# Kernel optimization log

Hardware: AMD Instinct MI355X
Metric: run time of the kernel (lower is better)

The kernel has to match this reference:

```python
import jax, jax.numpy as jnp
import numpy as np

H = 512      # hidden_size
NH = 8       # head_size (num heads)
DH = H // NH # att_size per head
FFN = 2048
B, S = 8, 1024
NEG = -1e9
EPS = 1e-5


def _layernorm(x, g, b):
    mu = jnp.mean(x, axis=-1, keepdims=True)
    var = jnp.var(x, axis=-1, keepdims=True)
    return (x - mu) * jax.lax.rsqrt(var + EPS) * g + b


def setup_inputs() -> dict:
    key = jax.random.key(0)
    ks = jax.random.split(key, 16)
    s = 0.02
    return {
        "x": jax.random.normal(ks[0], (B, S, H), jnp.float32),
        "attn_bias": jax.random.normal(ks[1], (B, S, S), jnp.float32),
        "graph_mask": jax.random.randint(ks[2], (B, S, S), 0, 2, jnp.int32),
        "ln1_g": jnp.ones((H,), jnp.float32),
        "ln1_b": jnp.zeros((H,), jnp.float32),
        "Wq": jax.random.normal(ks[3], (H, H), jnp.float32) * s,
        "bq": jnp.zeros((H,), jnp.float32),
        "Wk": jax.random.normal(ks[4], (H, H), jnp.float32) * s,
        "bk": jnp.zeros((H,), jnp.float32),
        "Wv": jax.random.normal(ks[5], (H, H), jnp.float32) * s,
        "bv": jnp.zeros((H,), jnp.float32),
        "Wo": jax.random.normal(ks[6], (H, H), jnp.float32) * s,
        "bo": jnp.zeros((H,), jnp.float32),
        "ln2_g": jnp.ones((H,), jnp.float32),
        "ln2_b": jnp.zeros((H,), jnp.float32),
        "W1": jax.random.normal(ks[7], (H, FFN), jnp.float32) * s,
        "b1": jnp.zeros((FFN,), jnp.float32),
        "W2": jax.random.normal(ks[8], (FFN, H), jnp.float32) * s,
        "b2": jnp.zeros((H,), jnp.float32),
    }


def reference(x, attn_bias, graph_mask, ln1_g, ln1_b, Wq, bq, Wk, bk, Wv, bv,
              Wo, bo, ln2_g, ln2_b, W1, b1, W2, b2):
    b, s, h = x.shape
    # --- self-attention block (eval mode: dropouts are identity) ---
    y = _layernorm(x, ln1_g, ln1_b)
    q = (y @ Wq + bq).reshape(b, s, NH, DH).transpose(0, 2, 1, 3)  # [B,h,S,d]
    k = (y @ Wk + bk).reshape(b, s, NH, DH).transpose(0, 2, 1, 3)
    v = (y @ Wv + bv).reshape(b, s, NH, DH).transpose(0, 2, 1, 3)
    scale = DH ** -0.5
    scores = jnp.einsum('bhqd,bhkd->bhqk', q * scale, k)  # [B,h,S,S]
    mask = (graph_mask == 0)[:, None, :, :]               # [B,1,S,S] broadcast over heads
    bias = jnp.where(mask, NEG, attn_bias[:, None, :, :])
    scores = scores + bias
    scores = jnp.where(mask, NEG, scores)
    p = jax.nn.softmax(scores, axis=-1)
    o = jnp.einsum('bhqk,bhkd->bhqd', p, v)
    o = o.transpose(0, 2, 1, 3).reshape(b, s, h) @ Wo + bo
    x = x + o
    # --- FFN block ---
    y = _layernorm(x, ln2_g, ln2_b)
    y = jax.nn.gelu(y @ W1 + b1, approximate=False) @ W2 + b2
    return x + y
```

## Files before the change

### kernel.cpp

```cpp
#include <hip/hip_runtime.h>
#include <hip/hip_bf16.h>
#include <type_traits>

static constexpr int kS   = 1024;
static constexpr int kH   = 512;
static constexpr int kFFN = 2048;

using bf16 = __hip_bfloat16;
using short8  = __attribute__((ext_vector_type(8))) short;
using float4v = __attribute__((ext_vector_type(4))) float;
#define MFMA16 __builtin_amdgcn_mfma_f32_16x16x32_bf16

__device__ __forceinline__ unsigned short f2bfu(float f){
  unsigned int u = __float_as_uint(f);
  return (unsigned short)((u + 0x7fffu + ((u >> 16) & 1u)) >> 16);
}
__device__ __forceinline__ float bfu2f(unsigned short u){
  return __uint_as_float(((unsigned int)u) << 16);
}
__device__ __forceinline__ unsigned int pack2(float a, float b){
  return (unsigned int)f2bfu(a) | ((unsigned int)f2bfu(b) << 16);
}
__device__ __forceinline__ void async16(const void* g, void* l){
  __builtin_amdgcn_global_load_lds(
    (const __attribute__((address_space(1))) unsigned int*)g,
    (__attribute__((address_space(3))) unsigned int*)l, 16, 0, 0);
}
__device__ __forceinline__ int swz(int col, int row){
  return (col & ~63) | (((((col>>3)&7) ^ (row&7)))<<3) | (col&7);
}

__device__ __forceinline__ void ln_row(const float* __restrict__ x,
    const float* __restrict__ g, const float* __restrict__ bb,
    bf16* __restrict__ y, long row, int lane){
  const float* xr = x + row * kH + lane*8;
  float4 a = *(const float4*)xr, c = *(const float4*)(xr+4);
  float v[8] = {a.x,a.y,a.z,a.w,c.x,c.y,c.z,c.w};
  float s=0.f, s2=0.f;
#pragma unroll
  for(int i=0;i<8;i++){ s += v[i]; s2 += v[i]*v[i]; }
#pragma unroll
  for(int o=32; o>=1; o>>=1){ s += __shfl_xor(s,o,64); s2 += __shfl_xor(s2,o,64); }
  float mu  = s * (1.f/kH);
  float rs  = rsqrtf(s2*(1.f/kH) - mu*mu + 1e-5f);
  float gv[8], bv[8];
  {
    float4 t0=*(const float4*)(g+lane*8),  t1=*(const float4*)(g+lane*8+4);
    float4 t2=*(const float4*)(bb+lane*8), t3=*(const float4*)(bb+lane*8+4);
    gv[0]=t0.x;gv[1]=t0.y;gv[2]=t0.z;gv[3]=t0.w;gv[4]=t1.x;gv[5]=t1.y;gv[6]=t1.z;gv[7]=t1.w;
    bv[0]=t2.x;bv[1]=t2.y;bv[2]=t2.z;bv[3]=t2.w;bv[4]=t3.x;bv[5]=t3.y;bv[6]=t3.z;bv[7]=t3.w;
  }
  unsigned int ow[4];
#pragma unroll
  for(int i=0;i<4;i++){
    float a0 = (v[2*i]  -mu)*rs*gv[2*i]   + bv[2*i];
    float a1 = (v[2*i+1]-mu)*rs*gv[2*i+1] + bv[2*i+1];
    ow[i] = pack2(a0, a1);
  }
  *reinterpret_cast<uint4*>(y + row*kH + swz(lane*8, (int)row)) = make_uint4(ow[0],ow[1],ow[2],ow[3]);
}

__global__ __launch_bounds__(256) void ln_kernel(const float* __restrict__ x,
    const float* __restrict__ g, const float* __restrict__ bb, bf16* __restrict__ y){
  ln_row(x, g, bb, y, (long)blockIdx.x*4 + (threadIdx.x>>6), threadIdx.x&63);
}

__device__ __forceinline__ void prep_tile(const float* __restrict__ W,
    bf16* __restrict__ WT, int K, int N, int kb, int nb){
  __shared__ unsigned short Ts[64*68];
  int tid=threadIdx.x;
  {
    int k=tid>>2, nc=(tid&3)*16;
    const float* p = W + (size_t)(kb+k)*N + nb+nc;
#pragma unroll
    for(int i=0;i<16;i+=4){
      float4 f = *(const float4*)(p+i);
      Ts[k*68+nc+i  ]=f2bfu(f.x); Ts[k*68+nc+i+1]=f2bfu(f.y);
      Ts[k*68+nc+i+2]=f2bfu(f.z); Ts[k*68+nc+i+3]=f2bfu(f.w);
    }
  }
  __syncthreads();
  {
    int n=tid>>2, kc=(tid&3)*16;
    unsigned short tmp[16];
#pragma unroll
    for(int i=0;i<16;i++) tmp[i] = Ts[(kc+i)*68 + n];
    int row = nb+n, kg0 = kc>>3;
    bf16* op = WT + (size_t)row*K + kb;
    *(uint4*)(op + (((kg0  ^(row&7)))<<3)) = *(uint4*)&tmp[0];
    *(uint4*)(op + ((((kg0+1)^(row&7)))<<3)) = *(uint4*)&tmp[8];
  }
}

__global__ __launch_bounds__(256) void ln1_prep_qkv(
    const float* __restrict__ x, const float* __restrict__ g, const float* __restrict__ bb,
    bf16* __restrict__ y, const float* __restrict__ Wq, const float* __restrict__ Wk,
    const float* __restrict__ Wv, bf16* __restrict__ WT){
  int id = blockIdx.x;
  if(id < 2048){
    ln_row(x, g, bb, y, (long)id*4 + (threadIdx.x>>6), threadIdx.x&63);
  } else {
    int pid = id - 2048, sel = pid>>6, lid = pid&63;
    const float* W = sel==0 ? Wq : (sel==1 ? Wk : Wv);
    prep_tile(W, WT + (size_t)sel*262144, kH, kH, (lid>>3)*64, (lid&7)*64);
  }
}

__global__ __launch_bounds__(256) void prep_rest(
    const float* __restrict__ Wo, const float* __restrict__ W1, const float* __restrict__ W2,
    bf16* __restrict__ WoT, bf16* __restrict__ W1T, bf16* __restrict__ W2T){
  int id = blockIdx.x;
  const float* W; bf16* WT; int K, N, kb, nb;
  if(id < 64)       { W=Wo; WT=WoT; K=kH;   N=kH;   kb=(id>>3)*64;        nb=(id&7)*64; }
  else if(id < 320) { int l=id-64;  W=W1; WT=W1T; K=kH;   N=kFFN; kb=(l>>5)*64; nb=(l&31)*64; }
  else              { int l=id-320; W=W2; WT=W2T; K=kFFN; N=kH;   kb=(l>>3)*64; nb=(l&7)*64; }
  prep_tile(W, WT, K, N, kb, nb);
}

__global__ __launch_bounds__(256) void bias_eff_kernel(
    const int* __restrict__ mask, const float* __restrict__ bias, bf16* __restrict__ be){
  size_t i8 = ((size_t)blockIdx.x*256 + threadIdx.x)*8;
  int4   m0 = *(const int4*)(mask+i8),   m1 = *(const int4*)(mask+i8+4);
  float4 b0 = *(const float4*)(bias+i8), b1 = *(const float4*)(bias+i8+4);
  const unsigned short NEG = f2bfu(-1e9f);
  unsigned short o[8];
  o[0]=m0.x?f2bfu(b0.x):NEG; o[1]=m0.y?f2bfu(b0.y):NEG;
  o[2]=m0.z?f2bfu(b0.z):NEG; o[3]=m0.w?f2bfu(b0.w):NEG;
  o[4]=m1.x?f2bfu(b1.x):NEG; o[5]=m1.y?f2bfu(b1.y):NEG;
  o[6]=m1.z?f2bfu(b1.z):NEG; o[7]=m1.w?f2bfu(b1.w):NEG;
  *(uint4*)((unsigned short*)be + i8) = *(uint4*)o;
}

__global__ __launch_bounds__(256, 4) void quad_gemm(
    const bf16* __restrict__ A, const bf16* __restrict__ BT,
    const float* __restrict__ bias, const float* __restrict__ res,
    float* __restrict__ C, int M, int N, int K)
{
  __shared__ __align__(16) unsigned short As[2][64*64];
  __shared__ __align__(16) unsigned short Bs[2][64*64];
  int tid=threadIdx.x, lane=tid&63, quad=lane>>4, l16=lane&15;
  int w=__builtin_amdgcn_readfirstlane(tid>>6);
  int wr=w>>1, wc=w&1;
  int m0=blockIdx.y*64, n0=blockIdx.x*64;
  int lr=lane>>3, lc=lane&7;
  float4v acc[2][2]={};
  auto stage=[&](int k0,int bi){
#pragma unroll
    for(int i=0;i<2;i++){
      int r=(w*2+i)*8;
      async16(A  + (size_t)(m0+r+lr)*K + k0 + lc*8, &As[bi][r*64]);
      async16(BT + (size_t)(n0+r+lr)*K + k0 + lc*8, &Bs[bi][r*64]);
    }
  };
  stage(0,0);
  __syncthreads();
  int NT = K>>6;
  for(int kt=0;kt<NT;kt++){
    int cur=kt&1;
    if(kt+1<NT) stage((kt+1)<<6, cur^1);
#pragma unroll
    for(int hf=0;hf<2;hf++){
      short8 af[2], bfv[2];
#pragma unroll
      for(int mi=0;mi<2;mi++){
        int row=wr*32+mi*16+l16;
        af[mi]=*(const short8*)&As[cur][row*64 + (((hf*4+quad)^(row&7))<<3)];
      }
#pragma unroll
      for(int ni=0;ni<2;ni++){
        int n=wc*32+ni*16+l16;
        bfv[ni]=*(const short8*)&Bs[cur][n*64 + (((hf*4+quad)^(n&7))<<3)];
      }
#pragma unroll
      for(int ni=0;ni<2;ni++)
#pragma unroll
        for(int mi=0;mi<2;mi++)
          acc[mi][ni]=MFMA16(af[mi],bfv[ni],acc[mi][ni],0,0,0);
    }
    __syncthreads();
  }
#pragma unroll
  for(int ni=0;ni<2;ni++){
    int col=n0+wc*32+ni*16+l16;
    float bc=bias[col];
#pragma unroll
    for(int mi=0;mi<2;mi++){
#pragma unroll
      for(int r=0;r<4;r++){
        int row=m0+wr*32+mi*16+quad*4+r;
        float v=acc[mi][ni][r]+bc;
        size_t idx=(size_t)row*N+col;
        v+=res[idx];
        C[idx]=v;
      }
    }
  }
}

__global__ __launch_bounds__(256, 4) void quad_gelu(
    const bf16* __restrict__ A, const bf16* __restrict__ BT,
    const float* __restrict__ bias, bf16* __restrict__ C, int M, int N, int K)
{
  __shared__ __align__(16) unsigned short As[2][64*64];
  __shared__ __align__(16) unsigned short Bs[2][64*64];
  int tid=threadIdx.x, lane=tid&63, quad=lane>>4, l16=lane&15;
  int w=__builtin_amdgcn_readfirstlane(tid>>6);
  int wr=w>>1, wc=w&1;
  int m0=blockIdx.y*64, n0=blockIdx.x*64;
  int lr=lane>>3, lc=lane&7;
  float4v acc[2][2]={};
  auto stage=[&](int k0,int bi){
#pragma unroll
    for(int i=0;i<2;i++){
      int r=(w*2+i)*8;
      async16(A  + (size_t)(m0+r+lr)*K + k0 + lc*8, &As[bi][r*64]);
      async16(BT + (size_t)(n0+r+lr)*K + k0 + lc*8, &Bs[bi][r*64]);
    }
  };
  stage(0,0);
  __syncthreads();
  int NT = K>>6;
  for(int kt=0;kt<NT;kt++){
    int cur=kt&1;
    if(kt+1<NT) stage((kt+1)<<6, cur^1);
#pragma unroll
    for(int hf=0;hf<2;hf++){
      short8 af[2], bfv[2];
#pragma unroll
      for(int mi=0;mi<2;mi++){
        int row=wr*32+mi*16+l16;
        af[mi]=*(const short8*)&As[cur][row*64 + (((hf*4+quad)^(row&7))<<3)];
      }
#pragma unroll
      for(int ni=0;ni<2;ni++){
        int n=wc*32+ni*16+l16;
        bfv[ni]=*(const short8*)&Bs[cur][n*64 + (((hf*4+quad)^(n&7))<<3)];
      }
#pragma unroll
      for(int ni=0;ni<2;ni++)
#pragma unroll
        for(int mi=0;mi<2;mi++)
          acc[mi][ni]=MFMA16(af[mi],bfv[ni],acc[mi][ni],0,0,0);
    }
    __syncthreads();
  }
#pragma unroll
  for(int ni=0;ni<2;ni++){
    int col=n0+wc*32+ni*16+l16;
    float bc=bias[col];
#pragma unroll
    for(int mi=0;mi<2;mi++){
#pragma unroll
      for(int r=0;r<4;r++){
        int row=m0+wr*32+mi*16+quad*4+r;
        float v=acc[mi][ni][r]+bc;
        v=0.5f*v*(1.f+erff(v*0.70710678118f));
        reinterpret_cast<unsigned short*>(C)[(size_t)row*N + swz(col,row)]=f2bfu(v);
      }
    }
  }
}

__global__ __launch_bounds__(256, 3) void mfma_gemm_qkv(
    const bf16* __restrict__ A, const bf16* __restrict__ BT,
    const float* __restrict__ bq, const float* __restrict__ bk, const float* __restrict__ bv,
    bf16* __restrict__ qo, bf16* __restrict__ ko, bf16* __restrict__ vT, int M, int N, int K)
{
  __shared__ __align__(16) unsigned short As[128*64];
  __shared__ __align__(16) unsigned short Bs[128*64];
  int tid=threadIdx.x, lane=tid&63, quad=lane>>4, l16=lane&15;
  int w=__builtin_amdgcn_readfirstlane(tid>>6);
  int wr = w >> 1, wc = w & 1;
  int m0=blockIdx.y*128, n0=blockIdx.x*128;
  int lr=lane>>3, lc=lane&7;
  float4v acc[4][4] = {};
  for(int k0=0;k0<K;k0+=64){
    __syncthreads();
#pragma unroll
    for(int i=0;i<4;i++){
      int r = (w*4+i)*8;
      async16(A + (size_t)(m0+r+lr)*K + k0 + lc*8, &As[r*64]);
    }
#pragma unroll
    for(int i=0;i<4;i++){
      int r = (w*4+i)*8;
      async16(BT + (size_t)(n0+r+lr)*K + k0 + lc*8, &Bs[r*64]);
    }
    __syncthreads();
#pragma unroll
    for(int hf=0;hf<2;hf++){
      short8 af[4], bfv[4];
#pragma unroll
      for(int mi=0;mi<4;mi++){
        int row=wr*64+mi*16+l16;
        af[mi]=*(const short8*)&As[row*64 + (((hf*4+quad)^(row&7))<<3)];
      }
#pragma unroll
      for(int ni=0;ni<4;ni++){
        int n=wc*64+ni*16+l16;
        bfv[ni]=*(const short8*)&Bs[n*64 + (((hf*4+quad)^(n&7))<<3)];
      }
#pragma unroll
      for(int ni=0;ni<4;ni++)
#pragma unroll
        for(int mi=0;mi<4;mi++)
          acc[mi][ni]=MFMA16(af[mi],bfv[ni],acc[mi][ni],0,0,0);
    }
  }
  int sec = __builtin_amdgcn_readfirstlane(n0 >> 9);
  const float* bp = sec==0 ? bq : (sec==1 ? bk : bv);
  if(sec == 2){
#pragma unroll
    for(int ni=0;ni<4;ni++){
      int cl=(n0+wc*64+ni*16+l16)&511;
      float bc=bp[cl];
#pragma unroll
      for(int mi=0;mi<4;mi++){
        int row0=m0+wr*64+mi*16+quad*4;
        unsigned int p0=pack2(acc[mi][ni][0]+bc, acc[mi][ni][1]+bc);
        unsigned int p1=pack2(acc[mi][ni][2]+bc, acc[mi][ni][3]+bc);
        *reinterpret_cast<uint2*>(reinterpret_cast<unsigned short*>(vT)
            + (size_t)cl*8192 + row0) = make_uint2(p0,p1);
      }
    }
  } else {
    unsigned short* dst = (unsigned short*)(sec==0 ? qo : ko);
    float scl = (sec==0) ? 0.125f : 1.0f;
#pragma unroll
    for(int ni=0;ni<4;ni++){
      int col=n0+wc*64+ni*16+l16, cl=col&511;
      float bc=bp[cl];
#pragma unroll
      for(int mi=0;mi<4;mi++){
#pragma unroll
        for(int r=0;r<4;r++){
          int row=m0+wr*64+mi*16+quad*4+r;
          dst[(size_t)row*512+cl]=f2bfu((acc[mi][ni][r]+bc)*scl);
        }
      }
    }
  }
}

__global__ __launch_bounds__(256,2) void attn_mfma(
    const bf16* __restrict__ q, const bf16* __restrict__ k,
    const bf16* __restrict__ vT, const bf16* __restrict__ be,
    bf16* __restrict__ o)
{
  __shared__ __align__(16) unsigned short Ks[2][64*64];
  __shared__ __align__(16) unsigned short Vt[2][64*64];
  __shared__ __align__(16) unsigned short Ps[4*32*72];
  int tid=threadIdx.x, lane=tid&63, quad=lane>>4, l16=lane&15;
  int w=__builtin_amdgcn_readfirstlane(tid>>6);
  int lin = blockIdx.x;
  int nid = (lin&7)*64 + (lin>>3);
  int q0=(nid&7)*128, bh=nid>>3, b=bh>>3, h=bh&7;
  int lr=lane>>3, lc=lane&7;
  short8 aq[2][2];
#pragma unroll
  for(int g=0;g<2;g++){
    const bf16* qp = q + (size_t)(b*kS + q0 + w*32 + g*16 + l16)*kH + h*64;
    aq[g][0] = *(const short8*)(qp + quad*8);
    aq[g][1] = *(const short8*)(qp + 32 + quad*8);
  }
  float lpart[2][4]={};
  float4v oacc[2][4]={};
  int pb = w*32*72;
  const unsigned short* beRow[2][4];
#pragma unroll
  for(int g=0;g<2;g++)
#pragma unroll
    for(int r=0;r<4;r++)
      beRow[g][r] = reinterpret_cast<const unsigned short*>(be)
                  + (size_t)(b*kS+q0+w*32+g*16+quad*4+r)*kS + l16;

  auto stage = [&](int kt, int bufi){
    int kb = kt*64;
#pragma unroll
    for(int i=0;i<2;i++){
      int rr = w*16 + i*8;
      async16(k  + (size_t)(b*kS+kb+rr+lr)*kH + h*64 + ((lc^lr)<<3), &Ks[bufi][rr*64]);
      async16(vT + (size_t)(h*64+rr+lr)*8192 + b*kS + kb + ((lc^lr)<<3), &Vt[bufi][rr*64]);
    }
  };
  float bevc[2][4][4];
  stage(0,0);
#pragma unroll
  for(int g=0;g<2;g++)
#pragma unroll
    for(int r=0;r<4;r++)
#pragma unroll
      for(int t=0;t<4;t++)
        bevc[g][r][t] = bfu2f(beRow[g][r][t*16]);
  __syncthreads();
  for(int kt=0;kt<16;kt++){
    int cur=kt&1;
    if(kt<15) stage(kt+1, cur^1);
    float4v sa[2][4];
#pragma unroll
    for(int t=0;t<4;t++){
      int krow=t*16+l16, kx=krow&7;
      short8 b0 = *(const short8*)&Ks[cur][krow*64 + ((quad^kx)<<3)];
      short8 b1 = *(const short8*)&Ks[cur][krow*64 + (((4+quad)^kx)<<3)];
#pragma unroll
      for(int g=0;g<2;g++){
        float4v ci;
#pragma unroll
        for(int r=0;r<4;r++) ci[r] = bevc[g][r][t];
        ci = MFMA16(aq[g][0],b0,ci,0,0,0);
        sa[g][t]=MFMA16(aq[g][1],b1,ci,0,0,0);
      }
    }
    if(kt<15){
      int kb2=(kt+1)*64;
#pragma unroll
      for(int g=0;g<2;g++)
#pragma unroll
        for(int r=0;r<4;r++)
#pragma unroll
          for(int t=0;t<4;t++)
            bevc[g][r][t] = bfu2f(beRow[g][r][kb2 + t*16]);
    }
#pragma unroll
    for(int g=0;g<2;g++)
#pragma unroll
    for(int t=0;t<4;t++){
      int kg = t*2 + (l16>>3), j = l16&7;
#pragma unroll
      for(int r=0;r<4;r++){
        float p = __expf(sa[g][t][r] - 24.f);
        lpart[g][r] += p;
        int row = g*16 + quad*4+r;
        Ps[pb + row*72 + ((kg^(row&7))<<3) + j] = f2bfu(p);
      }
    }
    short8 ap[2][2];
#pragma unroll
    for(int g=0;g<2;g++){
      int prow = g*16 + l16;
      ap[g][0] = *(const short8*)&Ps[pb + prow*72 + ((quad^(prow&7))<<3)];
      ap[g][1] = *(const short8*)&Ps[pb + prow*72 + (((4+quad)^(prow&7))<<3)];
    }
#pragma unroll
    for(int dt=0;dt<4;dt++){
      int vrow=dt*16+l16, vx=vrow&7;
      short8 bv0=*(const short8*)&Vt[cur][vrow*64+((quad^vx)<<3)];
      short8 bv1=*(const short8*)&Vt[cur][vrow*64+(((4+quad)^vx)<<3)];
#pragma unroll
      for(int g=0;g<2;g++){
        oacc[g][dt]=MFMA16(ap[g][0],bv0,oacc[g][dt],0,0,0);
        oacc[g][dt]=MFMA16(ap[g][1],bv1,oacc[g][dt],0,0,0);
      }
    }
    __syncthreads();
  }
#pragma unroll
  for(int g=0;g<2;g++){
    float inv[4];
#pragma unroll
    for(int r=0;r<4;r++){
      float l = lpart[g][r];
      l += __shfl_xor(l,1,64); l += __shfl_xor(l,2,64);
      l += __shfl_xor(l,4,64); l += __shfl_xor(l,8,64);
      inv[r] = 1.f/l;
    }
#pragma unroll
    for(int dt=0;dt<4;dt++)
#pragma unroll
      for(int r=0;r<4;r++){
        int row = b*kS + q0 + w*32 + g*16 + quad*4 + r;
        int col = h*64 + dt*16 + l16;
        reinterpret_cast<unsigned short*>(o)[(size_t)row*kH + swz(col,row)] =
          f2bfu(oacc[g][dt][r]*inv[r]);
      }
  }
}

extern "C" void kernel_launch(void* const* d_in, const int* in_sizes, int n_in,
                              void* d_out, int out_size, void* d_ws, size_t ws_size,
                              hipStream_t stream){
  (void)in_sizes; (void)n_in; (void)out_size; (void)ws_size;
  const float* x         = (const float*)d_in[0];
  const float* attn_bias = (const float*)d_in[1];
  const int*   graph_mask= (const int*)  d_in[2];
  const float* ln1_g = (const float*)d_in[3];
  const float* ln1_b = (const float*)d_in[4];
  const float* Wq = (const float*)d_in[5];
  const float* bq = (const float*)d_in[6];
  const float* Wk = (const float*)d_in[7];
  const float* bk = (const float*)d_in[8];
  const float* Wv = (const float*)d_in[9];
  const float* bv = (const float*)d_in[10];
  const float* Wo = (const float*)d_in[11];
  const float* bo = (const float*)d_in[12];
  const float* ln2_g = (const float*)d_in[13];
  const float* ln2_b = (const float*)d_in[14];
  const float* W1 = (const float*)d_in[15];
  const float* b1 = (const float*)d_in[16];
  const float* W2 = (const float*)d_in[17];
  const float* b2 = (const float*)d_in[18];

  char* wsb = (char*)d_ws;
  const size_t SZ = (size_t)8192 * kH * sizeof(bf16);
  bf16* s0 = (bf16*)(wsb);
  bf16* s1 = (bf16*)(wsb + SZ);
  bf16* s2 = (bf16*)(wsb + 2*SZ);
  bf16* s3 = (bf16*)(wsb + 3*SZ);
  float* outf = (float*)d_out;
  bf16*  WqkvT = (bf16*)d_out;
  bf16*  beP   = (bf16*)d_out;
  bf16* WoT = s3;
  bf16* W1T = s3 + 262144;
  bf16* W2T = s3 + 262144 + 1048576;

  dim3 blk(256);
  ln1_prep_qkv<<<dim3(2240), blk, 0, stream>>>(x, ln1_g, ln1_b, s0, Wq, Wk, Wv, WqkvT);
  mfma_gemm_qkv<<<dim3(12,64), blk, 0, stream>>>(s0, WqkvT, bq, bk, bv, s1, s2, s3, 8192, 3*kH, kH);
  bias_eff_kernel<<<dim3(4096), blk, 0, stream>>>(graph_mask, attn_bias, beP);
  attn_mfma<<<dim3(512), blk, 0, stream>>>(s1, s2, s3, beP, s0);
  prep_rest<<<dim3(576), blk, 0, stream>>>(Wo, W1, W2, WoT, W1T, W2T);
  quad_gemm<<<dim3(8,128), blk, 0, stream>>>(s0, WoT, bo, x, outf, 8192, kH, kH);
  ln_kernel<<<dim3(2048), blk, 0, stream>>>(outf, ln2_g, ln2_b, s0);
  for(int c=0;c<2;c++){
    size_t ro = (size_t)c * 4096 * kH;
    quad_gelu<<<dim3(32,64), blk, 0, stream>>>(s0 + ro, W1T, b1, s1, 4096, kFFN, kH);
    quad_gemm<<<dim3(8,64),  blk, 0, stream>>>(s1, W2T, b2, outf + ro, outf + ro, 4096, kH, kFFN);
  }
}
```

Before: 338.9 us.

## Shrink QKV and FFN2 GEMM tiles with double-buffered LDS for more blocks

The QKV projection moves from a single-buffered 128x128 tile kernel to a 64x64 tile kernel with double-buffered async LDS staging. This quadruples the grid and lets the next K-tile load overlap with the MFMAs. The FFN down-projection gets a new 32x64-tile kernel so its 4096-row chunks launch twice as many blocks, improving CU fill for the long K=2048 loop. The cost is less operand reuse per block and more global/L2 traffic for the B operand.

```diff
diff --git a/kernel.cpp b/kernel.cpp
--- a/kernel.cpp
+++ b/kernel.cpp
@@ -197,6 +197,61 @@
   }
 }
 
+__global__ __launch_bounds__(256, 4) void quad32_gemm(
+    const bf16* __restrict__ A, const bf16* __restrict__ BT,
+    const float* __restrict__ bias, const float* __restrict__ res,
+    float* __restrict__ C, int M, int N, int K)
+{
+  __shared__ __align__(16) unsigned short As[2][32*64];
+  __shared__ __align__(16) unsigned short Bs[2][64*64];
+  int tid=threadIdx.x, lane=tid&63, quad=lane>>4, l16=lane&15;
+  int w=__builtin_amdgcn_readfirstlane(tid>>6);
+  int wr=w>>1, wc=w&1;
+  int m0=blockIdx.y*32, n0=blockIdx.x*64;
+  int lr=lane>>3, lc=lane&7;
+  float4v acc[2]={};
+  auto stage=[&](int k0,int bi){
+#pragma unroll
+    for(int i=0;i<3;i++){
+      int g=w*3+i;
+      if(g<4) async16(A  + (size_t)(m0+g*8+lr)*K     + k0 + lc*8, &As[bi][g*8*64]);
+      else    async16(BT + (size_t)(n0+(g-4)*8+lr)*K + k0 + lc*8, &Bs[bi][(g-4)*8*64]);
+    }
+  };
+  stage(0,0);
+  __syncthreads();
+  int NT = K>>6;
+  for(int kt=0;kt<NT;kt++){
+    int cur=kt&1;
+    if(kt+1<NT) stage((kt+1)<<6, cur^1);
+#pragma unroll
+    for(int hf=0;hf<2;hf++){
+      int row=wr*16+l16;
+      short8 af=*(const short8*)&As[cur][row*64 + (((hf*4+quad)^(row&7))<<3)];
+#pragma unroll
+      for(int ni=0;ni<2;ni++){
+        int n=wc*32+ni*16+l16;
+        short8 bfv=*(const short8*)&Bs[cur][n*64 + (((hf*4+quad)^(n&7))<<3)];
+        acc[ni]=MFMA16(af,bfv,acc[ni],0,0,0);
+      }
+    }
+    __syncthreads();
+  }
+#pragma unroll
+  for(int ni=0;ni<2;ni++){
+    int col=n0+wc*32+ni*16+l16;
+    float bc=bias[col];
+#pragma unroll
+    for(int r=0;r<4;r++){
+      int row=m0+wr*16+quad*4+r;
+      float v=acc[ni][r]+bc;
+      size_t idx=(size_t)row*N+col;
+      v+=res[idx];
+      C[idx]=v;
+    }
+  }
+}
+
 __global__ __launch_bounds__(256, 4) void quad_gelu(
     const bf16* __restrict__ A, const bf16* __restrict__ BT,
     const float* __restrict__ bias, bf16* __restrict__ C, int M, int N, int K)
@@ -261,62 +316,64 @@
   }
 }
 
-__global__ __launch_bounds__(256, 3) void mfma_gemm_qkv(
+__global__ __launch_bounds__(256, 4) void quad_qkv(
     const bf16* __restrict__ A, const bf16* __restrict__ BT,
     const float* __restrict__ bq, const float* __restrict__ bk, const float* __restrict__ bv,
     bf16* __restrict__ qo, bf16* __restrict__ ko, bf16* __restrict__ vT, int M, int N, int K)
 {
-  __shared__ __align__(16) unsigned short As[128*64];
-  __shared__ __align__(16) unsigned short Bs[128*64];
+  __shared__ __align__(16) unsigned short As[2][64*64];
+  __shared__ __align__(16) unsigned short Bs[2][64*64];
   int tid=threadIdx.x, lane=tid&63, quad=lane>>4, l16=lane&15;
   int w=__builtin_amdgcn_readfirstlane(tid>>6);
-  int wr = w >> 1, wc = w & 1;
-  int m0=blockIdx.y*128, n0=blockIdx.x*128;
+  int wr=w>>1, wc=w&1;
+  int m0=blockIdx.y*64, n0=blockIdx.x*64;
   int lr=lane>>3, lc=lane&7;
-  float4v acc[4][4] = {};
-  for(int k0=0;k0<K;k0+=64){
+  float4v acc[2][2]={};
+  auto stage=[&](int k0,int bi){
+#pragma unroll
+    for(int i=0;i<2;i++){
+      int r=(w*2+i)*8;
+      async16(A  + (size_t)(m0+r+lr)*K + k0 + lc*8, &As[bi][r*64]);
+      async16(BT + (size_t)(n0+r+lr)*K + k0 + lc*8, &Bs[bi][r*64]);
+    }
+  };
+  stage(0,0);
+  __syncthreads();
+  int NT = K>>6;
+  for(int kt=0;kt<NT;kt++){
+    int cur=kt&1;
+    if(kt+1<NT) stage((kt+1)<<6, cur^1);
+#pragma unroll
+    for(int hf=0;hf<2;hf++){
+      short8 af[2], bfv[2];
+#pragma unroll
+      for(int mi=0;mi<2;mi++){
+        int row=wr*32+mi*16+l16;
+        af[mi]=*(const short8*)&As[cur][row*64 + (((hf*4+quad)^(row&7))<<3)];
+      }
+#pragma unroll
+      for(int ni=0;ni<2;ni++){
+        int n=wc*32+ni*16+l16;
+        bfv[ni]=*(const short8*)&Bs[cur][n*64 + (((hf*4+quad)^(n&7))<<3)];
+      }
+#pragma unroll
+      for(int ni=0;ni<2;ni++)
+#pragma unroll
+        for(int mi=0;mi<2;mi++)
+          acc[mi][ni]=MFMA16(af[mi],bfv[ni],acc[mi][ni],0,0,0);
+    }
     __syncthreads();
-#pragma unroll
-    for(int i=0;i<4;i++){
-      int r = (w*4+i)*8;
-      async16(A + (size_t)(m0+r+lr)*K + k0 + lc*8, &As[r*64]);
-    }
-#pragma unroll
-    for(int i=0;i<4;i++){
-      int r = (w*4+i)*8;
-      async16(BT + (size_t)(n0+r+lr)*K + k0 + lc*8, &Bs[r*64]);
-    }
-    __syncthreads();
-#pragma unroll
-    for(int hf=0;hf<2;hf++){
-      short8 af[4], bfv[4];
-#pragma unroll
-      for(int mi=0;mi<4;mi++){
-        int row=wr*64+mi*16+l16;
-        af[mi]=*(const short8*)&As[row*64 + (((hf*4+quad)^(row&7))<<3)];
-      }
-#pragma unroll
-      for(int ni=0;ni<4;ni++){
-        int n=wc*64+ni*16+l16;
-        bfv[ni]=*(const short8*)&Bs[n*64 + (((hf*4+quad)^(n&7))<<3)];
-      }
-#pragma unroll
-      for(int ni=0;ni<4;ni++)
-#pragma unroll
-        for(int mi=0;mi<4;mi++)
-          acc[mi][ni]=MFMA16(af[mi],bfv[ni],acc[mi][ni],0,0,0);
-    }
-  }
-  int sec = __builtin_amdgcn_readfirstlane(n0 >> 9);
+  }
+  int sec = __builtin_amdgcn_readfirstlane((int)blockIdx.x >> 3);
   const float* bp = sec==0 ? bq : (sec==1 ? bk : bv);
   if(sec == 2){
 #pragma unroll
-    for(int ni=0;ni<4;ni++){
-      int cl=(n0+wc*64+ni*16+l16)&511;
+    for(int ni=0;ni<2;ni++){
+      int cl=(n0+wc*32+ni*16+l16)&511;
       float bc=bp[cl];
 #pragma unroll
-      for(int mi=0;mi<4;mi++){
-        int row0=m0+wr*64+mi*16+quad*4;
+      for(int mi=0;mi<2;mi++){
+        int row0=m0+wr*32+mi*16+quad*4;
         unsigned int p0=pack2(acc[mi][ni][0]+bc, acc[mi][ni][1]+bc);
         unsigned int p1=pack2(acc[mi][ni][2]+bc, acc[mi][ni][3]+bc);
         *reinterpret_cast<uint2*>(reinterpret_cast<unsigned short*>(vT)
@@ -327,14 +384,14 @@
     unsigned short* dst = (unsigned short*)(sec==0 ? qo : ko);
     float scl = (sec==0) ? 0.125f : 1.0f;
 #pragma unroll
-    for(int ni=0;ni<4;ni++){
-      int col=n0+wc*64+ni*16+l16, cl=col&511;
+    for(int ni=0;ni<2;ni++){
+      int col=n0+wc*32+ni*16+l16, cl=col&511;
       float bc=bp[cl];
 #pragma unroll
-      for(int mi=0;mi<4;mi++){
+      for(int mi=0;mi<2;mi++){
 #pragma unroll
         for(int r=0;r<4;r++){
-          int row=m0+wr*64+mi*16+quad*4+r;
+          int row=m0+wr*32+mi*16+quad*4+r;
           dst[(size_t)row*512+cl]=f2bfu((acc[mi][ni][r]+bc)*scl);
         }
       }
@@ -515,7 +572,7 @@
 
   dim3 blk(256);
   ln1_prep_qkv<<<dim3(2240), blk, 0, stream>>>(x, ln1_g, ln1_b, s0, Wq, Wk, Wv, WqkvT);
-  mfma_gemm_qkv<<<dim3(12,64), blk, 0, stream>>>(s0, WqkvT, bq, bk, bv, s1, s2, s3, 8192, 3*kH, kH);
+  quad_qkv<<<dim3(24,128), blk, 0, stream>>>(s0, WqkvT, bq, bk, bv, s1, s2, s3, 8192, 3*kH, kH);
   bias_eff_kernel<<<dim3(4096), blk, 0, stream>>>(graph_mask, attn_bias, beP);
   attn_mfma<<<dim3(512), blk, 0, stream>>>(s1, s2, s3, beP, s0);
   prep_rest<<<dim3(576), blk, 0, stream>>>(Wo, W1, W2, WoT, W1T, W2T);
@@ -523,7 +580,7 @@
   ln_kernel<<<dim3(2048), blk, 0, stream>>>(outf, ln2_g, ln2_b, s0);
   for(int c=0;c<2;c++){
     size_t ro = (size_t)c * 4096 * kH;
-    quad_gelu<<<dim3(32,64), blk, 0, stream>>>(s0 + ro, W1T, b1, s1, 4096, kFFN, kH);
-    quad_gemm<<<dim3(8,64),  blk, 0, stream>>>(s1, W2T, b2, outf + ro, outf + ro, 4096, kH, kFFN);
-  }
-}
+    quad_gelu <<<dim3(32,64),  blk, 0, stream>>>(s0 + ro, W1T, b1, s1, 4096, kFFN, kH);
+    quad32_gemm<<<dim3(8,128), blk, 0, stream>>>(s1, W2T, b2, outf + ro, outf + ro, 4096, kH, kFFN);
+  }
+}
```

Result: faster. 331.0 us (-2.4%).
